# Kernel optimization log

Hardware: AMD Instinct MI355X
Metric: run time of the kernel (lower is better)

Reference implementation:

```python
import jax, jax.numpy as jnp
import numpy as np

B, CIN, HID, COUT, D, L = 2, 32, 64, 32, 20, 3
D2 = 2 * D
C4, C2 = COUT // 4, COUT // 2


def _conv3(x, W, b):
    # dense stride-1 'SAME' conv == MinkowskiConvolution on occupied set (background is 0)
    y = jax.lax.conv_general_dilated(x, W, (1, 1, 1), 'SAME',
                                     dimension_numbers=('NCDHW', 'OIDHW', 'NCDHW'))
    return y + b[None, :, None, None, None]


def _up(x, W, b):
    # generative conv-transpose, kernel 2 stride 2: out[:, :, 2i+p, 2j+q, 2k+r] = sum_c W[c,:,p,q,r] x[:,c,i,j,k]
    y = jnp.einsum('bcxyz,cdpqr->bdxpyqzr', x, W)
    y = y.reshape(x.shape[0], W.shape[1], 2 * x.shape[2], 2 * x.shape[3], 2 * x.shape[4])
    return y + b[None, :, None, None, None]


def _forward(x_feat, x_occ, target_occ, W_up, b_up, W_conv, b_conv,
             blk_W00, blk_b00, blk_W01, blk_b01, blk_W10, blk_b10,
             blk_W11, blk_b11, blk_W12, blk_b12, W_cls, b_cls, adaptive, rho=1.0):
    b = x_feat.shape[0]
    # occupancy of upsampled coords: every input voxel spawns its 2x2x2 children
    occ_up = jnp.repeat(jnp.repeat(jnp.repeat(x_occ, 2, 1), 2, 2), 2, 3)  # [B,D2,D2,D2]
    m = occ_up[:, None].astype(x_feat.dtype)
    out = jax.nn.relu(_up(x_feat, W_up, b_up) * m)
    out = jax.nn.relu(_conv3(out, W_conv, b_conv) * m)
    # InceptionResNet blocks (PCGCv2 style): two branches, concat, residual add
    for i in range(L):
        o0 = jax.nn.relu(_conv3(out, blk_W00[i], blk_b00[i]) * m)
        o0 = _conv3(o0, blk_W01[i], blk_b01[i]) * m
        o1 = jax.nn.relu(_conv3(out, blk_W10[i], blk_b10[i]) * m)
        o1 = jax.nn.relu(_conv3(o1, blk_W11[i], blk_b11[i]) * m)
        o1 = _conv3(o1, blk_W12[i], blk_b12[i]) * m
        out = jnp.concatenate([o0, o1], axis=1) + out
    out_cls = _conv3(out, W_cls, b_cls) * m
    # get_target_by_sp_tensor: isin(out coords, target coords) -> dense mask intersection
    occ_b = occ_up.astype(bool)
    target = occ_b & target_occ.astype(bool)
    # keep mask (computed under no_grad in torch)
    cls = jax.lax.stop_gradient(out_cls[:, 0]).reshape(b, -1)
    occ_flat = occ_b.reshape(b, -1)
    if adaptive:
        vals = jnp.where(occ_flat, cls, -jnp.inf)
        t_cnt = target_occ.astype(bool).reshape(b, -1).sum(-1)
        k = jnp.minimum(occ_flat.sum(-1), (t_cnt.astype(jnp.float32) * rho).astype(jnp.int32))
        order = jnp.argsort(-vals, axis=-1)
        ranks = jnp.argsort(order, axis=-1)   # descending rank of each voxel
        keep = (ranks < k[:, None]) & occ_flat
    else:
        keep = (cls > 0) & occ_flat
    keep = keep.reshape(occ_b.shape)
    keep = keep | target  # training mode: keep += target
    out_pruned = out * keep[:, None].astype(out.dtype)
    return out_pruned, out_cls, target, keep


def setup_inputs() -> dict:
    key = jax.random.key(0)
    ks = jax.random.split(key, 12)
    s = 0.05
    occ = jax.random.randint(ks[0], (B, D, D, D), 0, 2).astype(jnp.int32)
    x_feat = jax.random.normal(ks[1], (B, CIN, D, D, D), jnp.float32) * occ[:, None].astype(jnp.float32)
    target_occ = jax.random.randint(ks[2], (B, D2, D2, D2), 0, 2).astype(jnp.int32)
    return {
        'x_feat': x_feat, 'x_occ': occ, 'target_occ': target_occ,
        'W_up': jax.random.normal(ks[3], (CIN, HID, 2, 2, 2), jnp.float32) * s,
        'b_up': jnp.zeros((HID,), jnp.float32),
        'W_conv': jax.random.normal(ks[4], (COUT, HID, 3, 3, 3), jnp.float32) * s,
        'b_conv': jnp.zeros((COUT,), jnp.float32),
        'blk_W00': jax.random.normal(ks[5], (L, C4, COUT, 3, 3, 3), jnp.float32) * s,
        'blk_b00': jnp.zeros((L, C4), jnp.float32),
        'blk_W01': jax.random.normal(ks[6], (L, C2, C4, 3, 3, 3), jnp.float32) * s,
        'blk_b01': jnp.zeros((L, C2), jnp.float32),
        'blk_W10': jax.random.normal(ks[7], (L, C4, COUT, 1, 1, 1), jnp.float32) * s,
        'blk_b10': jnp.zeros((L, C4), jnp.float32),
        'blk_W11': jax.random.normal(ks[8], (L, C4, C4, 3, 3, 3), jnp.float32) * s,
        'blk_b11': jnp.zeros((L, C4), jnp.float32),
        'blk_W12': jax.random.normal(ks[9], (L, C2, C4, 1, 1, 1), jnp.float32) * s,
        'blk_b12': jnp.zeros((L, C2), jnp.float32),
        'W_cls': jax.random.normal(ks[10], (1, COUT, 3, 3, 3), jnp.float32) * s,
        'b_cls': jnp.zeros((1,), jnp.float32),
        'adaptive': 1,
    }


def reference(x_feat, x_occ, target_occ, W_up, b_up, W_conv, b_conv,
              blk_W00, blk_b00, blk_W01, blk_b01, blk_W10, blk_b10,
              blk_W11, blk_b11, blk_W12, blk_b12, W_cls, b_cls, adaptive):
    return _forward(x_feat, x_occ, target_occ, W_up, b_up, W_conv, b_conv,
                    blk_W00, blk_b00, blk_W01, blk_b01, blk_W10, blk_b10,
                    blk_W11, blk_b11, blk_W12, blk_b12, W_cls, b_cls, adaptive)
```

## Files before the change

kernel.cpp:

```cpp
#include <hip/hip_runtime.h>
#include <hip/hip_bf16.h>

#define S3 64000
#define NB 2

constexpr int OFF_WUP   = 0;
constexpr int OFF_WCONV = 16384;
constexpr int OFF_W00   = 71680;
constexpr int OFF_W01   = 92416;
constexpr int OFF_W10   = 102784;
constexpr int OFF_W11   = 103552;
constexpr int OFF_W12   = 108736;
constexpr int OFF_ZERO  = 109120;
constexpr int OFF_WCLS  = 109184;
constexpr int NPACK     = 110048;

__device__ const int g_offtab[27] = {
  -1641, -1640, -1639, -1601, -1600, -1599, -1561, -1560, -1559,
    -41,   -40,   -39,    -1,     0,     1,    39,    40,    41,
   1559,  1560,  1561,  1599,  1600,  1601,  1639,  1640,  1641
};

__device__ __forceinline__ int occ_at(const int* __restrict__ x_occ, int b, int s) {
  int d2 = s % 40; int t = s / 40; int d1 = t % 40; int d0 = t / 40;
  return x_occ[b * 8000 + (d0 >> 1) * 400 + (d1 >> 1) * 20 + (d2 >> 1)] != 0;
}

__device__ __forceinline__ unsigned int f2key(float f) {
  unsigned int u = __float_as_uint(f);
  return (u & 0x80000000u) ? ~u : (u | 0x80000000u);
}

__device__ __forceinline__ unsigned int edge_mask27(int d0, int d1, int d2) {
  unsigned int m = 0;
  #pragma unroll
  for (int k0 = 0; k0 < 3; ++k0)
  #pragma unroll
  for (int k1 = 0; k1 < 3; ++k1)
  #pragma unroll
  for (int k2 = 0; k2 < 3; ++k2) {
    bool ok = (k0 == 0 ? (d0 > 0) : (k0 == 2 ? (d0 < 39) : true))
           && (k1 == 0 ? (d1 > 0) : (k1 == 2 ? (d1 < 39) : true))
           && (k2 == 0 ? (d2 > 0) : (k2 == 2 ? (d2 < 39) : true));
    if (ok) m |= 1u << ((k0 * 3 + k1) * 3 + k2);
  }
  return m;
}

__global__ __launch_bounds__(256)
void pack_all(const float* __restrict__ Wup, const float* __restrict__ Wconv,
              const float* __restrict__ W00, const float* __restrict__ W01,
              const float* __restrict__ W10, const float* __restrict__ W11,
              const float* __restrict__ W12, const float* __restrict__ Wcls,
              float* __restrict__ wp) {
  int i = blockIdx.x * 256 + threadIdx.x;
  if (i < 16384) {
    int tap = i >> 11, rem = i & 2047, c = rem >> 6, d = rem & 63;
    wp[OFF_WUP + i] = Wup[((c << 6) | d) * 8 + tap];
    return;
  }
  i -= 16384;
  if (i < 55296) {
    int tap = i >> 11, c = (i >> 5) & 63, co = i & 31;
    wp[OFF_WCONV + i] = Wconv[(co * 64 + c) * 27 + tap];
    return;
  }
  i -= 55296;
  if (i < 20736) {
    int blk = i / 6912, r = i - blk * 6912;
    int tap = r >> 8, c = (r >> 3) & 31, co = r & 7;
    wp[OFF_W00 + i] = W00[((blk * 8 + co) * 32 + c) * 27 + tap];
    return;
  }
  i -= 20736;
  if (i < 10368) {
    int blk = i / 3456, r = i - blk * 3456;
    int tap = r >> 7, c = (r >> 4) & 7, co = r & 15;
    wp[OFF_W01 + i] = W01[((blk * 16 + co) * 8 + c) * 27 + tap];
    return;
  }
  i -= 10368;
  if (i < 768) {
    int blk = i / 256, r = i - blk * 256;
    int c = r >> 3, co = r & 7;
    wp[OFF_W10 + i] = W10[(blk * 8 + co) * 32 + c];
    return;
  }
  i -= 768;
  if (i < 5184) {
    int blk = i / 1728, r = i - blk * 1728;
    int tap = r >> 6, c = (r >> 3) & 7, co = r & 7;
    wp[OFF_W11 + i] = W11[((blk * 8 + co) * 8 + c) * 27 + tap];
    return;
  }
  i -= 5184;
  if (i < 384) {
    int blk = i / 128, r = i - blk * 128;
    int c = r >> 4, co = r & 15;
    wp[OFF_W12 + i] = W12[(blk * 16 + co) * 8 + c];
    return;
  }
  i -= 384;
  if (i < 64) { wp[OFF_ZERO + i] = 0.f; return; }
  i -= 64;
  if (i < 864) {
    int tap = i / 32, c = i % 32;
    wp[OFF_WCLS + i] = Wcls[c * 27 + tap];
  }
}

__global__ __launch_bounds__(64)
void up_kernel(const float* __restrict__ xf, const float* __restrict__ wup,
               const float* __restrict__ bup, const int* __restrict__ x_occ,
               float* __restrict__ outA) {
  int pv = blockIdx.x * 64 + threadIdx.x;
  int b = pv / 8000, p = pv - b * 8000;
  int p2 = p % 20, t = p / 20, p1 = t % 20, p0 = t / 20;
  int tap = blockIdx.y;
  int O0 = 2 * p0 + (tap >> 2), O1 = 2 * p1 + ((tap >> 1) & 1), O2 = 2 * p2 + (tap & 1);
  int s = O0 * 1600 + O1 * 40 + O2;
  float* op = outA + ((size_t)b * S3 + s) * 64;
  int occ = x_occ[pv];
  float4 z4 = make_float4(0.f, 0.f, 0.f, 0.f);
  if (!occ) {
    #pragma unroll
    for (int i = 0; i < 16; ++i) ((float4*)op)[i] = z4;
    return;
  }
  float acc[64];
  #pragma unroll
  for (int d = 0; d < 64; ++d) acc[d] = bup[d];
  const float* xb = xf + (size_t)b * 32 * 8000 + p;
  const float* wt = wup + tap * 2048;
  #pragma unroll 1
  for (int c = 0; c < 32; ++c) {
    float v = xb[c * 8000];
    const float* w = wt + c * 64;
    #pragma unroll
    for (int d = 0; d < 64; ++d) acc[d] = fmaf(v, w[d], acc[d]);
  }
  #pragma unroll
  for (int i = 0; i < 16; ++i)
    ((float4*)op)[i] = make_float4(fmaxf(acc[4*i],0.f), fmaxf(acc[4*i+1],0.f),
                                   fmaxf(acc[4*i+2],0.f), fmaxf(acc[4*i+3],0.f));
}

template<int CIN, int COUT, int WS, bool RELU>
__global__ __launch_bounds__(256)
void conv3_cl(const float* __restrict__ in, const float* __restrict__ w,
              const float* __restrict__ bias, const int* __restrict__ x_occ,
              const float* __restrict__ zpage, float* __restrict__ out, int outc) {
  int tid = blockIdx.x * 256 + threadIdx.x;
  int b = tid / S3, s = tid - b * S3;
  int d2 = s % 40; int t = s / 40; int d1 = t % 40; int d0 = t / 40;
  int occ = x_occ[b * 8000 + (d0 >> 1) * 400 + (d1 >> 1) * 20 + (d2 >> 1)];
  int cb = blockIdx.y * COUT;
  float* op = out + (size_t)tid * outc + cb;
  float4 z4 = make_float4(0.f, 0.f, 0.f, 0.f);
  if (!occ) {
    #pragma unroll
    for (int i = 0; i < COUT / 4; ++i) ((float4*)op)[i] = z4;
    return;
  }
  const float* wb = w + cb;
  const float* bb = bias + cb;
  float acc[COUT];
  #pragma unroll
  for (int c = 0; c < COUT; ++c) acc[c] = bb[c];
  const float* inb = in + (size_t)tid * CIN;
  unsigned int m27 = edge_mask27(d0, d1, d2);
  #pragma unroll 2
  for (int tap = 0; tap < 27; ++tap) {
    const float* p = ((m27 >> tap) & 1) ? (inb + g_offtab[tap] * CIN) : zpage;
    const float* wt = wb + tap * CIN * WS;
    #pragma unroll
    for (int c4 = 0; c4 < CIN / 4; ++c4) {
      float4 v = ((const float4*)p)[c4];
      const float* wc = wt + c4 * 4 * WS;
      #pragma unroll
      for (int c = 0; c < COUT; ++c) acc[c] = fmaf(v.x, wc[c], acc[c]);
      #pragma unroll
      for (int c = 0; c < COUT; ++c) acc[c] = fmaf(v.y, wc[WS + c], acc[c]);
      #pragma unroll
      for (int c = 0; c < COUT; ++c) acc[c] = fmaf(v.z, wc[2 * WS + c], acc[c]);
      #pragma unroll
      for (int c = 0; c < COUT; ++c) acc[c] = fmaf(v.w, wc[3 * WS + c], acc[c]);
    }
  }
  #pragma unroll
  for (int c = 0; c < COUT; ++c) if (RELU) acc[c] = fmaxf(acc[c], 0.f);
  #pragma unroll
  for (int c = 0; c < COUT / 4; ++c)
    ((float4*)op)[c] = make_float4(acc[4*c], acc[4*c+1], acc[4*c+2], acc[4*c+3]);
}

__global__ __launch_bounds__(256)
void conv_k1(const float* __restrict__ in, const float* __restrict__ w3,
             const float* __restrict__ w1, const float* __restrict__ b3,
             const float* __restrict__ b1, const int* __restrict__ x_occ,
             const float* __restrict__ zpage, float* __restrict__ T0o,
             float* __restrict__ T1o) {
  int tid = blockIdx.x * 256 + threadIdx.x;
  int b = tid / S3, s = tid - b * S3;
  int d2 = s % 40; int t = s / 40; int d1 = t % 40; int d0 = t / 40;
  int occ = x_occ[b * 8000 + (d0 >> 1) * 400 + (d1 >> 1) * 20 + (d2 >> 1)];
  float* o0 = T0o + (size_t)tid * 8;
  float* o1 = T1o + (size_t)tid * 8;
  float4 z4 = make_float4(0.f, 0.f, 0.f, 0.f);
  if (!occ) {
    ((float4*)o0)[0] = z4; ((float4*)o0)[1] = z4;
    ((float4*)o1)[0] = z4; ((float4*)o1)[1] = z4;
    return;
  }
  float a0[8], a1[8];
  #pragma unroll
  for (int co = 0; co < 8; ++co) { a0[co] = b3[co]; a1[co] = b1[co]; }
  const float* inb = in + (size_t)tid * 32;
  #pragma unroll
  for (int c4 = 0; c4 < 8; ++c4) {
    float4 v = ((const float4*)inb)[c4];
    const float* wc = w1 + c4 * 4 * 8;
    #pragma unroll
    for (int co = 0; co < 8; ++co) a1[co] = fmaf(v.x, wc[co], a1[co]);
    #pragma unroll
    for (int co = 0; co < 8; ++co) a1[co] = fmaf(v.y, wc[8 + co], a1[co]);
    #pragma unroll
    for (int co = 0; co < 8; ++co) a1[co] = fmaf(v.z, wc[16 + co], a1[co]);
    #pragma unroll
    for (int co = 0; co < 8; ++co) a1[co] = fmaf(v.w, wc[24 + co], a1[co]);
  }
  unsigned int m27 = edge_mask27(d0, d1, d2);
  #pragma unroll 2
  for (int tap = 0; tap < 27; ++tap) {
    const float* p = ((m27 >> tap) & 1) ? (inb + g_offtab[tap] * 32) : zpage;
    const float* wt = w3 + tap * 32 * 8;
    #pragma unroll
    for (int c4 = 0; c4 < 8; ++c4) {
      float4 v = ((const float4*)p)[c4];
      const float* wc = wt + c4 * 4 * 8;
      #pragma unroll
      for (int co = 0; co < 8; ++co) a0[co] = fmaf(v.x, wc[co], a0[co]);
      #pragma unroll
      for (int co = 0; co < 8; ++co) a0[co] = fmaf(v.y, wc[8 + co], a0[co]);
      #pragma unroll
      for (int co = 0; co < 8; ++co) a0[co] = fmaf(v.z, wc[16 + co], a0[co]);
      #pragma unroll
      for (int co = 0; co < 8; ++co) a0[co] = fmaf(v.w, wc[24 + co], a0[co]);
    }
  }
  ((float4*)o0)[0] = make_float4(fmaxf(a0[0],0.f), fmaxf(a0[1],0.f), fmaxf(a0[2],0.f), fmaxf(a0[3],0.f));
  ((float4*)o0)[1] = make_float4(fmaxf(a0[4],0.f), fmaxf(a0[5],0.f), fmaxf(a0[6],0.f), fmaxf(a0[7],0.f));
  ((float4*)o1)[0] = make_float4(fmaxf(a1[0],0.f), fmaxf(a1[1],0.f), fmaxf(a1[2],0.f), fmaxf(a1[3],0.f));
  ((float4*)o1)[1] = make_float4(fmaxf(a1[4],0.f), fmaxf(a1[5],0.f), fmaxf(a1[6],0.f), fmaxf(a1[7],0.f));
}

__global__ __launch_bounds__(256)
void conv_k3f(const float* __restrict__ t0, const float* __restrict__ t1,
              const float* __restrict__ resid, const float* __restrict__ w01,
              const float* __restrict__ w11, const float* __restrict__ w12,
              const float* __restrict__ bb01, const float* __restrict__ bb11,
              const float* __restrict__ bb12, const int* __restrict__ x_occ,
              const float* __restrict__ zpage, float* __restrict__ nxt) {
  int tid = blockIdx.x * 256 + threadIdx.x;
  int b = tid / S3, s = tid - b * S3;
  int d2 = s % 40; int t = s / 40; int d1 = t % 40; int d0 = t / 40;
  int occ = x_occ[b * 8000 + (d0 >> 1) * 400 + (d1 >> 1) * 20 + (d2 >> 1)];
  float* op = nxt + (size_t)tid * 32;
  float4 z4 = make_float4(0.f, 0.f, 0.f, 0.f);
  if (!occ) {
    #pragma unroll
    for (int i = 0; i < 8; ++i) ((float4*)op)[i] = z4;
    return;
  }
  float a[16], t2[8];
  #pragma unroll
  for (int co = 0; co < 16; ++co) a[co] = bb01[co];
  #pragma unroll
  for (int co = 0; co < 8; ++co) t2[co] = bb11[co];
  const float* t0b = t0 + (size_t)tid * 8;
  const float* t1b = t1 + (size_t)tid * 8;
  unsigned int m27 = edge_mask27(d0, d1, d2);
  #pragma unroll 2
  for (int tap = 0; tap < 27; ++tap) {
    bool ok = (m27 >> tap) & 1;
    const float* p0 = ok ? (t0b + g_offtab[tap] * 8) : zpage;
    const float* p1 = ok ? (t1b + g_offtab[tap] * 8) : zpage;
    const float* wt0 = w01 + tap * 128;
    #pragma unroll
    for (int c4 = 0; c4 < 2; ++c4) {
      float4 v = ((const float4*)p0)[c4];
      const float* wc = wt0 + c4 * 64;
      #pragma unroll
      for (int co = 0; co < 16; ++co) a[co] = fmaf(v.x, wc[co], a[co]);
      #pragma unroll
      for (int co = 0; co < 16; ++co) a[co] = fmaf(v.y, wc[16 + co], a[co]);
      #pragma unroll
      for (int co = 0; co < 16; ++co) a[co] = fmaf(v.z, wc[32 + co], a[co]);
      #pragma unroll
      for (int co = 0; co < 16; ++co) a[co] = fmaf(v.w, wc[48 + co], a[co]);
    }
    const float* wt1 = w11 + tap * 64;
    #pragma unroll
    for (int c4 = 0; c4 < 2; ++c4) {
      float4 v = ((const float4*)p1)[c4];
      const float* wc = wt1 + c4 * 32;
      #pragma unroll
      for (int co = 0; co < 8; ++co) t2[co] = fmaf(v.x, wc[co], t2[co]);
      #pragma unroll
      for (int co = 0; co < 8; ++co) t2[co] = fmaf(v.y, wc[8 + co], t2[co]);
      #pragma unroll
      for (int co = 0; co < 8; ++co) t2[co] = fmaf(v.z, wc[16 + co], t2[co]);
      #pragma unroll
      for (int co = 0; co < 8; ++co) t2[co] = fmaf(v.w, wc[24 + co], t2[co]);
    }
  }
  #pragma unroll
  for (int co = 0; co < 8; ++co) t2[co] = fmaxf(t2[co], 0.f);
  float a1[16];
  #pragma unroll
  for (int co = 0; co < 16; ++co) a1[co] = bb12[co];
  #pragma unroll
  for (int c = 0; c < 8; ++c) {
    #pragma unroll
    for (int co = 0; co < 16; ++co) a1[co] = fmaf(t2[c], w12[c * 16 + co], a1[co]);
  }
  const float* rb = resid + (size_t)tid * 32;
  float o[32];
  #pragma unroll
  for (int co = 0; co < 16; ++co) { o[co] = a[co]; o[16 + co] = a1[co]; }
  #pragma unroll
  for (int q = 0; q < 8; ++q) {
    float4 r = ((const float4*)rb)[q];
    o[4*q] += r.x; o[4*q+1] += r.y; o[4*q+2] += r.z; o[4*q+3] += r.w;
  }
  #pragma unroll
  for (int q = 0; q < 8; ++q)
    ((float4*)op)[q] = make_float4(o[4*q], o[4*q+1], o[4*q+2], o[4*q+3]);
}

__global__ __launch_bounds__(256)
void cls_kernel(const float* __restrict__ in, const float* __restrict__ w,
                const float* __restrict__ bias, const int* __restrict__ x_occ,
                const float* __restrict__ zpage, float* __restrict__ CLSo) {
  int tid = blockIdx.x * 256 + threadIdx.x;
  int b = tid / S3, s = tid - b * S3;
  int d2 = s % 40; int t = s / 40; int d1 = t % 40; int d0 = t / 40;
  int occ = x_occ[b * 8000 + (d0 >> 1) * 400 + (d1 >> 1) * 20 + (d2 >> 1)];
  if (!occ) { CLSo[tid] = 0.f; return; }
  float acc = bias[0];
  const float* inb = in + (size_t)tid * 32;
  unsigned int m27 = edge_mask27(d0, d1, d2);
  #pragma unroll 2
  for (int tap = 0; tap < 27; ++tap) {
    const float* p = ((m27 >> tap) & 1) ? (inb + g_offtab[tap] * 32) : zpage;
    const float* wt = w + tap * 32;
    #pragma unroll
    for (int c4 = 0; c4 < 8; ++c4) {
      float4 v = ((const float4*)p)[c4];
      acc = fmaf(v.x, wt[4*c4], acc);
      acc = fmaf(v.y, wt[4*c4+1], acc);
      acc = fmaf(v.z, wt[4*c4+2], acc);
      acc = fmaf(v.w, wt[4*c4+3], acc);
    }
  }
  CLSo[tid] = acc;
}

__global__ __launch_bounds__(256)
void sel_zero(int* __restrict__ hist) {
  int i = blockIdx.x * 256 + threadIdx.x;
  int n = 3 * NB * 65536 + NB * 16;
  for (int j = i; j < n; j += 512 * 256) hist[j] = 0;
}

__global__ __launch_bounds__(256)
void sel_hist1(const float* __restrict__ cls, const int* __restrict__ x_occ,
               const int* __restrict__ tgt, unsigned int* __restrict__ key,
               int* __restrict__ hist, int* __restrict__ sel) {
  int tid = blockIdx.x * 256 + threadIdx.x;
  int b = tid / S3, s = tid - b * S3;
  int occ = occ_at(x_occ, b, s);
  int tg = tgt[tid] != 0;
  unsigned int kk = occ ? f2key(cls[tid]) : 0u;
  key[tid] = kk;
  if (occ) atomicAdd(&hist[b * 65536 + (kk >> 16)], 1);
  unsigned long long bo = __ballot(occ);
  unsigned long long bt = __ballot(tg);
  if ((threadIdx.x & 63) == 0) {
    atomicAdd(&sel[b * 16 + 0], (int)__popcll(bo));
    atomicAdd(&sel[b * 16 + 1], (int)__popcll(bt));
  }
}

__global__ __launch_bounds__(256)
void sel_hist2(const unsigned int* __restrict__ key, const int* __restrict__ x_occ,
               int* __restrict__ hist, const int* __restrict__ sel) {
  int tid = blockIdx.x * 256 + threadIdx.x;
  int b = tid / S3, s = tid - b * S3;
  int B1 = sel[b * 16 + 4];
  if (B1 < 0) return;
  if (!occ_at(x_occ, b, s)) return;
  unsigned int kk = key[tid];
  if ((int)(kk >> 16) == B1) atomicAdd(&hist[(NB + b) * 65536 + (kk & 0xFFFFu)], 1);
}

__global__ __launch_bounds__(256)
void sel_hist3(const unsigned int* __restrict__ key, const int* __restrict__ x_occ,
               int* __restrict__ hist, const int* __restrict__ sel) {
  int tid = blockIdx.x * 256 + threadIdx.x;
  int b = tid / S3, s = tid - b * S3;
  int B1 = sel[b * 16 + 4];
  if (B1 < 0) return;
  if (!occ_at(x_occ, b, s)) return;
  unsigned int k32 = ((unsigned)B1 << 16) | (unsigned)sel[b * 16 + 5];
  if (key[tid] == k32) atomicAdd(&hist[(2 * NB + b) * 65536 + (65535 - s)], 1);
}

__global__ __launch_bounds__(256)
void sel_scan(int* __restrict__ hist, int* __restrict__ sel,
              const int* __restrict__ adaptive_flag, int phase) {
  int b = blockIdx.x;
  int* sb = sel + b * 16;
  __shared__ int chunk[256];
  __shared__ int s_active, s_rank;
  int t = threadIdx.x;
  if (t == 0) {
    int active = 1;
    if (phase == 0) {
      int k = min(sb[0], sb[1]);
      sb[2] = k; sb[3] = k;
      if (!adaptive_flag[0] || k == 0) {
        sb[4] = -1000000;
        *(unsigned long long*)(sb + 6) = ~0ull;
        active = 0;
      }
    } else if (sb[4] == -1000000) {
      active = 0;
    }
    s_active = active; s_rank = sb[3];
  }
  __syncthreads();
  if (!s_active) return;
  const int* hb = hist + (phase * NB + b) * 65536;
  int sum = 0;
  #pragma unroll 4
  for (int v = 0; v < 256; ++v) sum += hb[t * 256 + v];
  chunk[t] = sum;
  __syncthreads();
  if (t == 0) {
    int r = s_rank, acc = 0, C = 0;
    for (int c = 255; c >= 0; --c) {
      if (acc + chunk[c] >= r) { C = c; r -= acc; break; }
      acc += chunk[c];
    }
    int B = C * 256;
    acc = 0;
    for (int v = 255; v >= 0; --v) {
      int h = hb[C * 256 + v];
      if (acc + h >= r) { B = C * 256 + v; r -= acc; break; }
      acc += h;
    }
    if (phase == 0)      { sb[4] = B; sb[3] = r; }
    else if (phase == 1) { sb[5] = B; sb[3] = r; }
    else {
      unsigned long long T = ((unsigned long long)sb[4] << 16) | (unsigned)sb[5];
      T = (T << 16) | (unsigned)B;
      *(unsigned long long*)(sb + 6) = T;
    }
  }
}

__global__ __launch_bounds__(256)
void emit_prune(const float* __restrict__ cls, const unsigned int* __restrict__ key,
                const int* __restrict__ x_occ, const int* __restrict__ tgt,
                const int* __restrict__ adaptive_flag, const int* __restrict__ sel,
                const float* __restrict__ cur, float* __restrict__ dout) {
  int tid = blockIdx.x * 256 + threadIdx.x;
  int b = tid / S3, s = tid - b * S3;
  int occ = occ_at(x_occ, b, s);
  int tg = occ && (tgt[tid] != 0);
  float c = cls[tid];
  bool kp;
  if (adaptive_flag[0]) {
    unsigned long long T = *(const unsigned long long*)(sel + b * 16 + 6);
    unsigned long long k48 = ((unsigned long long)key[tid] << 16) | (unsigned)(65535 - s);
    kp = occ && (k48 >= T);
  } else {
    kp = occ && (c > 0.f);
  }
  kp = kp || tg;
  float* tail = dout + (size_t)NB * 32 * S3;
  tail[tid] = c;
  tail[NB * S3 + tid] = tg ? 1.f : 0.f;
  tail[2 * NB * S3 + tid] = kp ? 1.f : 0.f;
  float sc = kp ? 1.f : 0.f;
  const float4* ip = (const float4*)(cur + (size_t)tid * 32);
  float* ob = dout + (size_t)b * 32 * S3 + s;
  #pragma unroll
  for (int i = 0; i < 8; ++i) {
    float4 q = ip[i];
    ob[(4 * i) * S3] = q.x * sc; ob[(4 * i + 1) * S3] = q.y * sc;
    ob[(4 * i + 2) * S3] = q.z * sc; ob[(4 * i + 3) * S3] = q.w * sc;
  }
}

extern "C" void kernel_launch(void* const* d_in, const int* in_sizes, int n_in,
                              void* d_out, int out_size, void* d_ws, size_t ws_size,
                              hipStream_t stream) {
  const float* x_feat    = (const float*)d_in[0];
  const int*   x_occ     = (const int*)d_in[1];
  const int*   target_oc = (const int*)d_in[2];
  const float* W_up   = (const float*)d_in[3];
  const float* b_up   = (const float*)d_in[4];
  const float* W_conv = (const float*)d_in[5];
  const float* b_conv = (const float*)d_in[6];
  const float* W00 = (const float*)d_in[7];
  const float* b00 = (const float*)d_in[8];
  const float* W01 = (const float*)d_in[9];
  const float* b01 = (const float*)d_in[10];
  const float* W10 = (const float*)d_in[11];
  const float* b10 = (const float*)d_in[12];
  const float* W11 = (const float*)d_in[13];
  const float* b11 = (const float*)d_in[14];
  const float* W12 = (const float*)d_in[15];
  const float* b12 = (const float*)d_in[16];
  const float* W_cls = (const float*)d_in[17];
  const float* b_cls = (const float*)d_in[18];
  const int*   adaptive = (const int*)d_in[19];

  float* ws = (float*)d_ws;
  float* wp = ws;
  float* zp = wp + OFF_ZERO;
  float* A  = ws + (1 << 17);
  float* B0 = A + (size_t)NB * S3 * 64;
  float* B1 = B0 + (size_t)NB * S3 * 32;
  float* T0 = A;
  float* T1 = T0 + (size_t)NB * S3 * 8;
  float* CLS = T1 + (size_t)NB * S3 * 8;
  unsigned int* KEY = (unsigned int*)(CLS + (size_t)NB * S3);
  int* HIST = (int*)(KEY + (size_t)NB * S3);
  int* SEL  = HIST + 3 * NB * 65536;

  float* outf = (float*)d_out;

  pack_all<<<(NPACK + 255) / 256, 256, 0, stream>>>(W_up, W_conv, W00, W01, W10, W11, W12, W_cls, wp);
  up_kernel<<<dim3(250, 8), 64, 0, stream>>>(x_feat, wp + OFF_WUP, b_up, x_occ, A);
  conv3_cl<64, 16, 32, true><<<dim3(500, 2), 256, 0, stream>>>(A, wp + OFF_WCONV, b_conv, x_occ, zp, B0, 32);

  float* cur = B0;
  float* nxt = B1;
  for (int i = 0; i < 3; ++i) {
    conv_k1<<<500, 256, 0, stream>>>(cur, wp + OFF_W00 + i * 6912, wp + OFF_W10 + i * 256,
                                     b00 + i * 8, b10 + i * 8, x_occ, zp, T0, T1);
    conv_k3f<<<500, 256, 0, stream>>>(T0, T1, cur, wp + OFF_W01 + i * 3456, wp + OFF_W11 + i * 1728,
                                      wp + OFF_W12 + i * 128, b01 + i * 16, b11 + i * 8, b12 + i * 16,
                                      x_occ, zp, nxt);
    float* tswap = cur; cur = nxt; nxt = tswap;
  }
  cls_kernel<<<500, 256, 0, stream>>>(cur, wp + OFF_WCLS, b_cls, x_occ, zp, CLS);

  sel_zero<<<512, 256, 0, stream>>>(HIST);
  sel_hist1<<<500, 256, 0, stream>>>(CLS, x_occ, target_oc, KEY, HIST, SEL);
  sel_scan<<<NB, 256, 0, stream>>>(HIST, SEL, adaptive, 0);
  sel_hist2<<<500, 256, 0, stream>>>(KEY, x_occ, HIST, SEL);
  sel_scan<<<NB, 256, 0, stream>>>(HIST, SEL, adaptive, 1);
  sel_hist3<<<500, 256, 0, stream>>>(KEY, x_occ, HIST, SEL);
  sel_scan<<<NB, 256, 0, stream>>>(HIST, SEL, adaptive, 2);
  emit_prune<<<500, 256, 0, stream>>>(CLS, KEY, x_occ, target_oc, adaptive, SEL, cur, outf);
}
```

Measured before the change: 641.4 us.

## Stage 3D halo tiles of branch inputs in LDS for fused 3x3x3 conv

The fused block conv kernel now maps each 256-thread block to an 8x8x4 spatial tile and cooperatively loads a 10x10x6 halo of both 8-channel branch inputs into shared memory, zero-filling out-of-bounds voxels. Each thread then reads its 27 neighbours from LDS using a halo offset table. This replaces the per-tap global gathers and the edge-mask/zero-page logic. The aim is to cut redundant global/L2 traffic for neighbour reads. In exchange it adds about 38 KB of LDS per block, which may limit occupancy, and loads the halo even for tiles that are largely unoccupied.

Measured after the change: 664.2 us. 3.6% more time.

```diff
diff --git a/kernel.cpp b/kernel.cpp
--- a/kernel.cpp
+++ b/kernel.cpp
@@ -19,6 +19,12 @@
   -1641, -1640, -1639, -1601, -1600, -1599, -1561, -1560, -1559,
     -41,   -40,   -39,    -1,     0,     1,    39,    40,    41,
    1559,  1560,  1561,  1599,  1600,  1601,  1639,  1640,  1641
+};
+
+__device__ const int g_hofftab[27] = {
+  -67, -66, -65, -61, -60, -59, -55, -54, -53,
+   -7,  -6,  -5,  -1,   0,   1,   5,   6,   7,
+   53,  54,  55,  59,  60,  61,  65,  66,  67
 };
 
 __device__ __forceinline__ int occ_at(const int* __restrict__ x_occ, int b, int s) {
@@ -260,31 +266,54 @@
               const float* __restrict__ w11, const float* __restrict__ w12,
               const float* __restrict__ bb01, const float* __restrict__ bb11,
               const float* __restrict__ bb12, const int* __restrict__ x_occ,
-              const float* __restrict__ zpage, float* __restrict__ nxt) {
-  int tid = blockIdx.x * 256 + threadIdx.x;
-  int b = tid / S3, s = tid - b * S3;
-  int d2 = s % 40; int t = s / 40; int d1 = t % 40; int d0 = t / 40;
+              float* __restrict__ nxt) {
+  __shared__ float sh0[600 * 8];
+  __shared__ float sh1[600 * 8];
+  int bid = blockIdx.x;
+  int b = bid / 250, tile = bid - b * 250;
+  int tt0 = tile / 50, tt1 = (tile / 10) % 5, tt2 = tile % 10;
+  int base0 = tt0 * 8, base1 = tt1 * 8, base2 = tt2 * 4;
+  for (int h = threadIdx.x; h < 600; h += 256) {
+    int h0 = h / 60, r = h - h0 * 60, h1 = r / 6, h2 = r - h1 * 6;
+    int g0 = base0 + h0 - 1, g1 = base1 + h1 - 1, g2 = base2 + h2 - 1;
+    bool in = ((unsigned)g0 < 40u) && ((unsigned)g1 < 40u) && ((unsigned)g2 < 40u);
+    float4 z4 = make_float4(0.f, 0.f, 0.f, 0.f);
+    float4 v0a = z4, v0b = z4, v1a = z4, v1b = z4;
+    if (in) {
+      size_t gs = ((size_t)b * S3 + g0 * 1600 + g1 * 40 + g2) * 8;
+      v0a = ((const float4*)(t0 + gs))[0];
+      v0b = ((const float4*)(t0 + gs))[1];
+      v1a = ((const float4*)(t1 + gs))[0];
+      v1b = ((const float4*)(t1 + gs))[1];
+    }
+    ((float4*)(sh0 + h * 8))[0] = v0a;
+    ((float4*)(sh0 + h * 8))[1] = v0b;
+    ((float4*)(sh1 + h * 8))[0] = v1a;
+    ((float4*)(sh1 + h * 8))[1] = v1b;
+  }
+  __syncthreads();
+  int t0i = threadIdx.x >> 5, t1i = (threadIdx.x >> 2) & 7, t2i = threadIdx.x & 3;
+  int d0 = base0 + t0i, d1 = base1 + t1i, d2 = base2 + t2i;
+  int s = d0 * 1600 + d1 * 40 + d2;
+  size_t tid = (size_t)b * S3 + s;
   int occ = x_occ[b * 8000 + (d0 >> 1) * 400 + (d1 >> 1) * 20 + (d2 >> 1)];
-  float* op = nxt + (size_t)tid * 32;
+  float* op = nxt + tid * 32;
   float4 z4 = make_float4(0.f, 0.f, 0.f, 0.f);
   if (!occ) {
     #pragma unroll
     for (int i = 0; i < 8; ++i) ((float4*)op)[i] = z4;
     return;
   }
-  float a[16], t2[8];
+  float a[16], t2r[8];
   #pragma unroll
   for (int co = 0; co < 16; ++co) a[co] = bb01[co];
   #pragma unroll
-  for (int co = 0; co < 8; ++co) t2[co] = bb11[co];
-  const float* t0b = t0 + (size_t)tid * 8;
-  const float* t1b = t1 + (size_t)tid * 8;
-  unsigned int m27 = edge_mask27(d0, d1, d2);
+  for (int co = 0; co < 8; ++co) t2r[co] = bb11[co];
+  int hc = (t0i + 1) * 60 + (t1i + 1) * 6 + (t2i + 1);
   #pragma unroll 2
   for (int tap = 0; tap < 27; ++tap) {
-    bool ok = (m27 >> tap) & 1;
-    const float* p0 = ok ? (t0b + g_offtab[tap] * 8) : zpage;
-    const float* p1 = ok ? (t1b + g_offtab[tap] * 8) : zpage;
+    const float* p0 = sh0 + (hc + g_hofftab[tap]) * 8;
+    const float* p1 = sh1 + (hc + g_hofftab[tap]) * 8;
     const float* wt0 = w01 + tap * 128;
     #pragma unroll
     for (int c4 = 0; c4 < 2; ++c4) {
@@ -305,26 +334,26 @@
       float4 v = ((const float4*)p1)[c4];
       const float* wc = wt1 + c4 * 32;
       #pragma unroll
-      for (int co = 0; co < 8; ++co) t2[co] = fmaf(v.x, wc[co], t2[co]);
-      #pragma unroll
-      for (int co = 0; co < 8; ++co) t2[co] = fmaf(v.y, wc[8 + co], t2[co]);
-      #pragma unroll
-      for (int co = 0; co < 8; ++co) t2[co] = fmaf(v.z, wc[16 + co], t2[co]);
-      #pragma unroll
-      for (int co = 0; co < 8; ++co) t2[co] = fmaf(v.w, wc[24 + co], t2[co]);
-    }
-  }
-  #pragma unroll
-  for (int co = 0; co < 8; ++co) t2[co] = fmaxf(t2[co], 0.f);
+      for (int co = 0; co < 8; ++co) t2r[co] = fmaf(v.x, wc[co], t2r[co]);
+      #pragma unroll
+      for (int co = 0; co < 8; ++co) t2r[co] = fmaf(v.y, wc[8 + co], t2r[co]);
+      #pragma unroll
+      for (int co = 0; co < 8; ++co) t2r[co] = fmaf(v.z, wc[16 + co], t2r[co]);
+      #pragma unroll
+      for (int co = 0; co < 8; ++co) t2r[co] = fmaf(v.w, wc[24 + co], t2r[co]);
+    }
+  }
+  #pragma unroll
+  for (int co = 0; co < 8; ++co) t2r[co] = fmaxf(t2r[co], 0.f);
   float a1[16];
   #pragma unroll
   for (int co = 0; co < 16; ++co) a1[co] = bb12[co];
   #pragma unroll
   for (int c = 0; c < 8; ++c) {
     #pragma unroll
-    for (int co = 0; co < 16; ++co) a1[co] = fmaf(t2[c], w12[c * 16 + co], a1[co]);
-  }
-  const float* rb = resid + (size_t)tid * 32;
+    for (int co = 0; co < 16; ++co) a1[co] = fmaf(t2r[c], w12[c * 16 + co], a1[co]);
+  }
+  const float* rb = resid + tid * 32;
   float o[32];
   #pragma unroll
   for (int co = 0; co < 16; ++co) { o[co] = a[co]; o[16 + co] = a1[co]; }
@@ -554,7 +583,7 @@
                                      b00 + i * 8, b10 + i * 8, x_occ, zp, T0, T1);
     conv_k3f<<<500, 256, 0, stream>>>(T0, T1, cur, wp + OFF_W01 + i * 3456, wp + OFF_W11 + i * 1728,
                                       wp + OFF_W12 + i * 128, b01 + i * 16, b11 + i * 8, b12 + i * 16,
-                                      x_occ, zp, nxt);
+                                      x_occ, nxt);
     float* tswap = cur; cur = nxt; nxt = tswap;
   }
   cls_kernel<<<500, 256, 0, stream>>>(cur, wp + OFF_WCLS, b_cls, x_occ, zp, CLS);
```
